# Optimization experiments

Hardware: AMD Instinct MI355X
Metric: run time of the kernel (lower is better)

The kernel has to match this reference:

```python
import jax, jax.numpy as jnp
import numpy as np

B, S, D, H, L, DFF, NA = 128, 52, 1024, 16, 8, 4096, 1000
DK = D // H
KTOP = int((1.0 - 0.9) * S)  # per-row top-k kept before threshold = 5
EPS = 1e-5
SCALE = 1.0 / np.sqrt(DK).astype(np.float32)


def setup_inputs() -> dict:
    key = jax.random.key(0)
    ks = jax.random.split(key, 30)
    # token grid: channels 0,1 in [0,50) so only designated positions match special tokens
    x = jax.random.randint(ks[0], (B, S, 3), 0, 50).astype(jnp.int32)
    act = jax.random.randint(ks[1], (B, S), 0, NA).astype(jnp.int32)
    x = x.at[..., 2].set(act)
    x = x.at[:, 0].set(jnp.array([100, 0, 1], jnp.int32))    # SOS
    x = x.at[:, 26].set(jnp.array([100, 0, 2], jnp.int32))   # SEP
    x = x.at[:, 48:].set(jnp.array([100, 0, 0], jnp.int32))  # PAD tail

    def n(k, shape, scale=0.02):
        return (jax.random.normal(k, shape) * scale).astype(jnp.float32)

    return dict(
        x=x,
        action_emb=n(ks[2], (NA, D), 1.0),
        sep_token=n(ks[3], (D,), 1.0),
        bn_gamma=jnp.ones((S,), jnp.float32),
        bn_beta=jnp.zeros((S,), jnp.float32),
        Wq=n(ks[4], (L, D, D)), bq=jnp.zeros((L, D), jnp.float32),
        Wk=n(ks[5], (L, D, D)), bk=jnp.zeros((L, D), jnp.float32),
        Wv=n(ks[6], (L, D, D)), bv=jnp.zeros((L, D), jnp.float32),
        Wo=n(ks[7], (L, D, D)), bo=jnp.zeros((L, D), jnp.float32),
        W1=n(ks[8], (L, DFF, D)), b1=jnp.zeros((L, DFF), jnp.float32),
        W2=n(ks[9], (L, D, DFF)), b2=jnp.zeros((L, D), jnp.float32),
        ln1_g=jnp.ones((L, D), jnp.float32), ln1_b=jnp.zeros((L, D), jnp.float32),
        ln2_g=jnp.ones((L, D), jnp.float32), ln2_b=jnp.zeros((L, D), jnp.float32),
        Wout=n(ks[10], (3, D)), bout=jnp.zeros((3,), jnp.float32),
    )


def _ln(x, g, b):
    m = x.mean(-1, keepdims=True)
    v = x.var(-1, keepdims=True)
    return (x - m) * jax.lax.rsqrt(v + EPS) * g + b


def reference(x, action_emb, sep_token, bn_gamma, bn_beta,
              Wq, bq, Wk, bk, Wv, bv, Wo, bo,
              W1, b1, W2, b2, ln1_g, ln1_b, ln2_g, ln2_b, Wout, bout):
    PAD = jnp.array([100, 0, 0], x.dtype)
    SEP = jnp.array([100, 0, 2], x.dtype)
    pad = jnp.all(x == PAD, -1)            # [B,S]
    sep = jnp.all(x == SEP, -1)            # [B,S]
    valid = ~pad                            # attend only to non-pad keys

    # token-scatter embedding: sep positions -> sep_token, everything else -> action embedding
    h = jnp.where(sep[..., None], sep_token, action_emb[x[..., 2]])  # [B,S,D]

    # BatchNorm1d(52) over seq-as-channel dim (training-mode batch stats)
    mu = h.mean((0, 2), keepdims=True)
    var = h.var((0, 2), keepdims=True)
    h = (h - mu) * jax.lax.rsqrt(var + EPS) * bn_gamma[None, :, None] + bn_beta[None, :, None]

    for l in range(L):
        q = (h @ Wq[l].T + bq[l]).reshape(B, S, H, DK).transpose(0, 2, 1, 3)
        k = (h @ Wk[l].T + bk[l]).reshape(B, S, H, DK).transpose(0, 2, 1, 3)
        v = (h @ Wv[l].T + bv[l]).reshape(B, S, H, DK).transpose(0, 2, 1, 3)
        scores = jnp.einsum('bhqd,bhkd->bhqk', q, k) * SCALE       # [B,H,S,S]
        scores = jnp.where(valid[:, None, None, :], scores, -1e9)
        thr = jax.lax.top_k(scores, KTOP)[0][..., -1:]              # per-row k-th largest
        sparse = scores * (scores >= thr).astype(scores.dtype)      # zero out sub-threshold
        attn = jax.nn.softmax(sparse, axis=-1)
        o = jnp.einsum('bhqk,bhkd->bhqd', attn, v).transpose(0, 2, 1, 3).reshape(B, S, D)
        o = o @ Wo[l].T + bo[l]
        h = _ln(h + o, ln1_g[l], ln1_b[l])
        f = jax.nn.relu(h @ W1[l].T + b1[l]) @ W2[l].T + b2[l]
        h = _ln(h + f, ln2_g[l], ln2_b[l])

    y = h @ Wout.T + bout                                           # [B,S,3]
    return y[:, -1]
```

## Files before the change

kernel.cpp:

```cpp
#include <hip/hip_runtime.h>
#include <cstddef>
#include <cstdint>

#define B_    128
#define S_    52
#define D_    1024
#define H_    16
#define L_    8
#define DFF_  4096
#define DK_   64
#define T_    (B_*S_)
#define EPS_  1e-5f
#define SCALE_ 0.125f

typedef unsigned short ushortx4 __attribute__((ext_vector_type(4)));
typedef short  bf16x8 __attribute__((ext_vector_type(8)));
typedef float  f32x4  __attribute__((ext_vector_type(4)));

__device__ __forceinline__ unsigned short f2b(float f) {
  unsigned int u = __builtin_bit_cast(unsigned int, f);
  u = u + 0x7fffu + ((u >> 16) & 1u);
  return (unsigned short)(u >> 16);
}
__device__ __forceinline__ float b2f(unsigned short b) {
  unsigned int u = ((unsigned int)b) << 16;
  return __builtin_bit_cast(float, u);
}
__device__ __forceinline__ void gload16(const void* g, void* l) {
  __builtin_amdgcn_global_load_lds((const __attribute__((address_space(1))) unsigned int*)g,
      (__attribute__((address_space(3))) unsigned int*)l, 16, 0, 0);
}

__global__ __launch_bounds__(256) void k_embed(const int* __restrict__ x,
    const float* __restrict__ aemb, const float* __restrict__ sept,
    float* __restrict__ h, float* __restrict__ part, int* __restrict__ mask)
{
  int row = blockIdx.x;
  int b = row / S_;
  int s = row - b * S_;
  const int* xr = x + (size_t)row * 3;
  int x0 = xr[0], x1 = xr[1], x2 = xr[2];
  bool issep = (x0 == 100) && (x1 == 0) && (x2 == 2);
  bool ispad = (x0 == 100) && (x1 == 0) && (x2 == 0);
  int t = threadIdx.x;
  if (t == 0) mask[row] = ispad ? 0 : 1;
  const float* src = issep ? sept : (aemb + (size_t)x2 * D_);
  size_t base = (size_t)row * D_;
  float s1 = 0.f, s2 = 0.f;
#pragma unroll
  for (int i = 0; i < 4; ++i) {
    int d = t + i * 256;
    float v = src[d];
    h[base + d] = v;
    s1 += v;
    s2 += v * v;
  }
#pragma unroll
  for (int off = 32; off; off >>= 1) {
    s1 += __shfl_down(s1, off);
    s2 += __shfl_down(s2, off);
  }
  __shared__ float red[8];
  int lane = t & 63, wid = t >> 6;
  if (lane == 0) { red[wid] = s1; red[4 + wid] = s2; }
  __syncthreads();
  if (t == 0) {
    part[(size_t)s * B_ + b]        = red[0] + red[1] + red[2] + red[3];
    part[(size_t)(S_ + s) * B_ + b] = red[4] + red[5] + red[6] + red[7];
  }
}

__global__ __launch_bounds__(128) void k_bn_reduce(const float* __restrict__ part,
                                                   float* __restrict__ stats)
{
  int s = blockIdx.x;
  int t = threadIdx.x;
  float s1 = part[(size_t)s * B_ + t];
  float s2 = part[(size_t)(S_ + s) * B_ + t];
#pragma unroll
  for (int off = 32; off; off >>= 1) {
    s1 += __shfl_down(s1, off);
    s2 += __shfl_down(s2, off);
  }
  __shared__ float red[4];
  int lane = t & 63, wid = t >> 6;
  if (lane == 0) { red[wid] = s1; red[2 + wid] = s2; }
  __syncthreads();
  if (t == 0) {
    stats[s]      = red[0] + red[1];
    stats[S_ + s] = red[2] + red[3];
  }
}

__global__ __launch_bounds__(256) void k_bn_apply(float* __restrict__ h,
    const float* __restrict__ stats, const float* __restrict__ g,
    const float* __restrict__ bb, unsigned short* __restrict__ hb)
{
  int row = blockIdx.x;
  int s = row % S_;
  const float cnt = (float)(B_ * D_);
  float mu  = stats[s] / cnt;
  float var = stats[S_ + s] / cnt - mu * mu;
  float sc  = rsqrtf(var + EPS_) * g[s];
  float off = bb[s] - mu * sc;
  size_t base = (size_t)row * D_;
  int t = threadIdx.x;
#pragma unroll
  for (int i = 0; i < 4; ++i) {
    int d = t + i * 256;
    float v = h[base + d] * sc + off;
    h[base + d] = v;
    hb[base + d] = f2b(v);
  }
}

__global__ __launch_bounds__(256) void k_wconv(
    const float* __restrict__ wq, const float* __restrict__ wk,
    const float* __restrict__ wv, const float* __restrict__ wo,
    const float* __restrict__ w1, const float* __restrict__ w2,
    unsigned short* __restrict__ out)
{
  const size_t DD = (size_t)D_ * D_;
  const size_t DF = (size_t)DFF_ * D_;
  const size_t total = 4 * DD + 2 * DF;
  size_t stride = (size_t)gridDim.x * 256 * 4;
  for (size_t i = ((size_t)blockIdx.x * 256 + threadIdx.x) * 4; i < total; i += stride) {
    const float* src; size_t off;
    if      (i < DD)          { src = wq; off = i; }
    else if (i < 2 * DD)      { src = wk; off = i - DD; }
    else if (i < 3 * DD)      { src = wv; off = i - 2 * DD; }
    else if (i < 4 * DD)      { src = wo; off = i - 3 * DD; }
    else if (i < 4 * DD + DF) { src = w1; off = i - 4 * DD; }
    else                      { src = w2; off = i - 4 * DD - DF; }
    float4 v = *reinterpret_cast<const float4*>(src + off);
    ushortx4 o = { f2b(v.x), f2b(v.y), f2b(v.z), f2b(v.w) };
    *reinterpret_cast<ushortx4*>(out + i) = o;
  }
}

__global__ __launch_bounds__(256) void k_bcat(const float* __restrict__ bq,
    const float* __restrict__ bk, const float* __restrict__ bv,
    float* __restrict__ out)
{
  int i = blockIdx.x * 256 + threadIdx.x;
  int l = i / 3072, j = i - l * 3072;
  float v = (j < D_) ? bq[l * D_ + j] : (j < 2 * D_) ? bk[l * D_ + j - D_]
                                                     : bv[l * D_ + j - 2 * D_];
  out[i] = v;
}

template<int RELU, int OUTBF16>
__global__ __launch_bounds__(512) void k_gemm8(
    const unsigned short* __restrict__ A, const unsigned short* __restrict__ Wt,
    const float* __restrict__ bias, void* __restrict__ C,
    int Mtiles, int Ntiles, int K, int ldc)
{
  __shared__ unsigned short lds[3 * 24576];
  const int tid = threadIdx.x;
  const int w = tid >> 6, l = tid & 63;

  const int nwg = Mtiles * Ntiles;
  int id = blockIdx.x;
  int swz = (id & 7) * (nwg >> 3) + (id >> 3);
  int bym = swz % Mtiles, bxn = swz / Mtiles;
  const int bm = bym * 256, bn = bxn * 128;

  const int srow = l >> 3;
  const unsigned inrow = ((l & 7) << 4) ^ ((l & 0x38) << 1);
  const char* gA = (const char*)A + (size_t)(bm + w * 32 + srow) * ((size_t)K * 2) + inrow;
  const char* gB = (const char*)Wt + (size_t)(bn + w * 16 + srow) * ((size_t)K * 2) + inrow;
  const size_t rj = (size_t)8 * K * 2;
  const int ldsA0 = w * 2048;
  const int ldsB0 = 16384 + w * 1024;

#define STAGE8(tt, bb) do {                                   \
    size_t kb = (size_t)(tt) * 128;                           \
    unsigned short* la = lds + (bb) * 24576 + ldsA0;          \
    unsigned short* lb = lds + (bb) * 24576 + ldsB0;          \
    gload16(gA + kb,          la);                            \
    gload16(gA + kb + rj,     la + 512);                      \
    gload16(gA + kb + 2 * rj, la + 1024);                     \
    gload16(gA + kb + 3 * rj, la + 1536);                     \
    gload16(gB + kb,          lb);                            \
    gload16(gB + kb + rj,     lb + 512);                      \
  } while (0)

  const int fr = l & 15, kg = l >> 4;
  const int wr = w >> 1, wcn = w & 1;
  const unsigned sw = (fr & 7) << 4;
  const unsigned colk0 = ((unsigned)(kg * 16)) ^ sw;
  const unsigned colk1 = ((unsigned)(64 + kg * 16)) ^ sw;
  const unsigned aRow0 = (unsigned)(wr * 64 + fr) * 128;
  const unsigned bRow0 = 32768u + (unsigned)(wcn * 64 + fr) * 128;

  f32x4 acc[4][4] = {};
  const int NT = K >> 6;

  STAGE8(0, 0);
  STAGE8(1, 1);
  asm volatile("s_waitcnt vmcnt(6)" ::: "memory");
  __builtin_amdgcn_sched_barrier(0);
  __builtin_amdgcn_s_barrier();
  __builtin_amdgcn_sched_barrier(0);

  int cur = 0;
  for (int t = 0; t < NT; ++t) {
    if (t + 2 < NT) {
      int sb = cur + 2; if (sb >= 3) sb -= 3;
      STAGE8(t + 2, sb);
    }
    const char* bp = (const char*)(lds + cur * 24576);
    bf16x8 bfr[4][2];
#pragma unroll
    for (int n = 0; n < 4; ++n) {
      bfr[n][0] = *(const bf16x8*)(bp + bRow0 + n * 2048 + colk0);
      bfr[n][1] = *(const bf16x8*)(bp + bRow0 + n * 2048 + colk1);
    }
#pragma unroll
    for (int m = 0; m < 4; ++m) {
      bf16x8 a0 = *(const bf16x8*)(bp + aRow0 + m * 2048 + colk0);
      bf16x8 a1 = *(const bf16x8*)(bp + aRow0 + m * 2048 + colk1);
#pragma unroll
      for (int n = 0; n < 4; ++n) {
        acc[m][n] = __builtin_amdgcn_mfma_f32_16x16x32_bf16(a0, bfr[n][0], acc[m][n], 0, 0, 0);
        acc[m][n] = __builtin_amdgcn_mfma_f32_16x16x32_bf16(a1, bfr[n][1], acc[m][n], 0, 0, 0);
      }
    }
    if (t + 1 < NT) {
      if (t + 2 < NT) { asm volatile("s_waitcnt vmcnt(6)" ::: "memory"); }
      else            { asm volatile("s_waitcnt vmcnt(0)" ::: "memory"); }
      __builtin_amdgcn_sched_barrier(0);
      __builtin_amdgcn_s_barrier();
      __builtin_amdgcn_sched_barrier(0);
    }
    cur = (cur == 2) ? 0 : cur + 1;
  }
#undef STAGE8

#pragma unroll
  for (int n = 0; n < 4; ++n) {
    int col = bn + wcn * 64 + n * 16 + fr;
    float bv = bias[col];
#pragma unroll
    for (int m = 0; m < 4; ++m) {
      int row0 = bm + wr * 64 + m * 16 + kg * 4;
#pragma unroll
      for (int j = 0; j < 4; ++j) {
        float v = acc[m][n][j] + bv;
        if (RELU) v = fmaxf(v, 0.f);
        if (OUTBF16)
          ((unsigned short*)C)[(size_t)(row0 + j) * ldc + col] = f2b(v);
        else
          ((float*)C)[(size_t)(row0 + j) * ldc + col] = v;
      }
    }
  }
}

__global__ __launch_bounds__(64) void k_attn(const unsigned short* __restrict__ qkv,
    const int* __restrict__ mask, unsigned short* __restrict__ ao)
{
  __shared__ float sc[64][68];
  __shared__ unsigned short ph[64][68];
  __shared__ unsigned short plo[64][68];
  __shared__ unsigned short vT[64][68];
  __shared__ float dnm[64];

  int blk = blockIdx.x;
  int b = blk >> 4, hh = blk & 15;
  int l = threadIdx.x;
  int cl = l & 15, kg = l >> 4;
  const unsigned short* base = qkv + (size_t)(b * S_) * 3072 + hh * 64;

  {
    const unsigned short* vp = base + 2048 + l;
#pragma unroll 4
    for (int k = 0; k < S_; ++k)
      vT[l][k] = vp[(size_t)k * 3072];
#pragma unroll
    for (int k = S_; k < 64; ++k) vT[l][k] = 0;
  }

  bf16x8 qa[4][2], kb[4][2];
#pragma unroll
  for (int mi = 0; mi < 4; ++mi) {
    int row = mi * 16 + cl;
    bool ok = (row < S_);
    const unsigned short* qp = base + (size_t)row * 3072 + kg * 8;
#pragma unroll
    for (int ks = 0; ks < 2; ++ks) {
      bf16x8 z = {};
      qa[mi][ks] = ok ? *reinterpret_cast<const bf16x8*>(qp + ks * 32) : z;
      kb[mi][ks] = ok ? *reinterpret_cast<const bf16x8*>(qp + 1024 + ks * 32) : z;
    }
  }

  f32x4 acc[4][4] = {};
#pragma unroll
  for (int ks = 0; ks < 2; ++ks)
#pragma unroll
    for (int mi = 0; mi < 4; ++mi)
#pragma unroll
      for (int ci = 0; ci < 4; ++ci)
        acc[mi][ci] = __builtin_amdgcn_mfma_f32_16x16x32_bf16(qa[mi][ks], kb[ci][ks], acc[mi][ci], 0, 0, 0);

  int vld[4];
#pragma unroll
  for (int ci = 0; ci < 4; ++ci) {
    int col = ci * 16 + cl;
    vld[ci] = (col < S_) ? mask[b * S_ + col] : 0;
  }
#pragma unroll
  for (int mi = 0; mi < 4; ++mi)
#pragma unroll
    for (int ci = 0; ci < 4; ++ci)
#pragma unroll
      for (int j = 0; j < 4; ++j)
        sc[mi * 16 + kg * 4 + j][ci * 16 + cl] = vld[ci] ? acc[mi][ci][j] * SCALE_ : -1e9f;

  __syncthreads();

  if (l < S_) {
    float v0 = -3e38f, v1 = -3e38f, v2 = -3e38f, v3 = -3e38f, v4 = -3e38f;
    const float4* rp = reinterpret_cast<const float4*>(&sc[l][0]);
#pragma unroll
    for (int c4 = 0; c4 < 13; ++c4) {
      float4 x = rp[c4];
      float xs[4] = { x.x, x.y, x.z, x.w };
#pragma unroll
      for (int u = 0; u < 4; ++u) {
        float xv = xs[u];
        if      (xv > v0) { v4 = v3; v3 = v2; v2 = v1; v1 = v0; v0 = xv; }
        else if (xv > v1) { v4 = v3; v3 = v2; v2 = v1; v1 = xv; }
        else if (xv > v2) { v4 = v3; v3 = v2; v2 = xv; }
        else if (xv > v3) { v4 = v3; v3 = xv; }
        else if (xv > v4) { v4 = xv; }
      }
    }
    float thr = v4;
    float m = fmaxf(v0, 0.f);
    float denom = 0.f;
    for (int c = 0; c < S_; ++c) {
      float xv = sc[l][c];
      float sp = (xv >= thr) ? xv : 0.f;
      float e = __expf(sp - m);
      denom += e;
      unsigned short hi = f2b(e);
      ph[l][c] = hi;
      plo[l][c] = f2b(e - b2f(hi));
    }
#pragma unroll
    for (int c = S_; c < 64; ++c) { ph[l][c] = 0; plo[l][c] = 0; }
    dnm[l] = 1.f / denom;
  }
  __syncthreads();

  f32x4 o[4][4] = {};
#pragma unroll
  for (int ks = 0; ks < 2; ++ks) {
    bf16x8 vf[4];
#pragma unroll
    for (int di = 0; di < 4; ++di)
      vf[di] = *reinterpret_cast<const bf16x8*>(&vT[di * 16 + cl][ks * 32 + kg * 8]);
#pragma unroll
    for (int mi = 0; mi < 4; ++mi) {
      bf16x8 ahi = *reinterpret_cast<const bf16x8*>(&ph[mi * 16 + cl][ks * 32 + kg * 8]);
      bf16x8 alo = *reinterpret_cast<const bf16x8*>(&plo[mi * 16 + cl][ks * 32 + kg * 8]);
#pragma unroll
      for (int di = 0; di < 4; ++di) {
        o[mi][di] = __builtin_amdgcn_mfma_f32_16x16x32_bf16(ahi, vf[di], o[mi][di], 0, 0, 0);
        o[mi][di] = __builtin_amdgcn_mfma_f32_16x16x32_bf16(alo, vf[di], o[mi][di], 0, 0, 0);
      }
    }
  }

#pragma unroll
  for (int mi = 0; mi < 4; ++mi) {
    int row = mi * 16 + kg * 4;
    if (row < S_) {
#pragma unroll
      for (int j = 0; j < 4; ++j) {
        int r = row + j;
        float inv = dnm[r];
        unsigned short* aop = ao + (size_t)(b * S_ + r) * D_ + hh * DK_;
#pragma unroll
        for (int di = 0; di < 4; ++di)
          aop[di * 16 + cl] = f2b(o[mi][di][j] * inv);
      }
    }
  }
}

__global__ __launch_bounds__(256) void k_add_ln(float* __restrict__ h,
    const float* __restrict__ r, const float* __restrict__ g,
    const float* __restrict__ bb, unsigned short* __restrict__ hb)
{
  int row = blockIdx.x;
  size_t base = (size_t)row * D_;
  int t = threadIdx.x;
  float xs[4];
  float s1 = 0.f, s2 = 0.f;
#pragma unroll
  for (int i = 0; i < 4; ++i) {
    int d = t + i * 256;
    float xv = h[base + d] + r[base + d];
    xs[i] = xv;
    s1 += xv;
    s2 += xv * xv;
  }
#pragma unroll
  for (int off = 32; off; off >>= 1) {
    s1 += __shfl_down(s1, off);
    s2 += __shfl_down(s2, off);
  }
  __shared__ float red[8];
  int lane = t & 63, wid = t >> 6;
  if (lane == 0) { red[wid] = s1; red[4 + wid] = s2; }
  __syncthreads();
  if (t == 0) {
    red[0] = red[0] + red[1] + red[2] + red[3];
    red[4] = red[4] + red[5] + red[6] + red[7];
  }
  __syncthreads();
  float mean = red[0] / (float)D_;
  float var  = red[4] / (float)D_ - mean * mean;
  float inv  = rsqrtf(var + EPS_);
#pragma unroll
  for (int i = 0; i < 4; ++i) {
    int d = t + i * 256;
    float v = (xs[i] - mean) * inv * g[d] + bb[d];
    h[base + d] = v;
    hb[base + d] = f2b(v);
  }
}

__global__ __launch_bounds__(256) void k_final(const float* __restrict__ h,
    const float* __restrict__ Wout, const float* __restrict__ bout,
    float* __restrict__ y)
{
  int b = blockIdx.x;
  const float* hr = h + (size_t)(b * S_ + (S_ - 1)) * D_;
  int t = threadIdx.x;
  float p0 = 0.f, p1 = 0.f, p2 = 0.f;
  for (int d = t; d < D_; d += 256) {
    float xv = hr[d];
    p0 += xv * Wout[d];
    p1 += xv * Wout[D_ + d];
    p2 += xv * Wout[2 * D_ + d];
  }
#pragma unroll
  for (int off = 32; off; off >>= 1) {
    p0 += __shfl_down(p0, off);
    p1 += __shfl_down(p1, off);
    p2 += __shfl_down(p2, off);
  }
  __shared__ float red[12];
  int lane = t & 63, wid = t >> 6;
  if (lane == 0) { red[wid] = p0; red[4 + wid] = p1; red[8 + wid] = p2; }
  __syncthreads();
  if (t == 0) {
    y[b * 3 + 0] = red[0] + red[1] + red[2]  + red[3]  + bout[0];
    y[b * 3 + 1] = red[4] + red[5] + red[6]  + red[7]  + bout[1];
    y[b * 3 + 2] = red[8] + red[9] + red[10] + red[11] + bout[2];
  }
}

extern "C" void kernel_launch(void* const* d_in, const int* in_sizes, int n_in,
                              void* d_out, int out_size, void* d_ws, size_t ws_size,
                              hipStream_t stream)
{
  const int*   x    = (const int*)d_in[0];
  const float* aemb = (const float*)d_in[1];
  const float* sept = (const float*)d_in[2];
  const float* bng  = (const float*)d_in[3];
  const float* bnb  = (const float*)d_in[4];
  const float* Wq = (const float*)d_in[5];  const float* bq = (const float*)d_in[6];
  const float* Wk = (const float*)d_in[7];  const float* bk = (const float*)d_in[8];
  const float* Wv = (const float*)d_in[9];  const float* bv = (const float*)d_in[10];
  const float* Wo = (const float*)d_in[11]; const float* bo = (const float*)d_in[12];
  const float* W1 = (const float*)d_in[13]; const float* b1 = (const float*)d_in[14];
  const float* W2 = (const float*)d_in[15]; const float* b2 = (const float*)d_in[16];
  const float* ln1g = (const float*)d_in[17]; const float* ln1b = (const float*)d_in[18];
  const float* ln2g = (const float*)d_in[19]; const float* ln2b = (const float*)d_in[20];
  const float* Wout = (const float*)d_in[21]; const float* bout = (const float*)d_in[22];
  float* out = (float*)d_out;

  float* ws = (float*)d_ws;
  const size_t TD = (size_t)T_ * D_;
  const size_t DD = (size_t)D_ * D_;
  const size_t DF = (size_t)DFF_ * D_;
  float* h   = ws;
  float* tmp = ws + TD;
  unsigned short* hb   = (unsigned short*)(ws + 2 * TD);
  unsigned short* qkvb = (unsigned short*)(ws + 2 * TD + TD / 2);
  unsigned short* aob  = (unsigned short*)(ws + 4 * TD);
  unsigned short* ffb  = (unsigned short*)(ws + 4 * TD + TD / 2);
  unsigned short* wbuf = (unsigned short*)(ws + 6 * TD + TD / 2);
  float* bqkv = ws + 6 * TD + TD / 2 + (4 * DD + 2 * DF) / 2;
  float* stats = bqkv + L_ * 3072;
  float* part  = stats + 2 * S_;
  int*   mask  = (int*)(part + 2 * S_ * B_);

  k_embed<<<T_, 256, 0, stream>>>(x, aemb, sept, h, part, mask);
  k_bn_reduce<<<S_, 128, 0, stream>>>(part, stats);
  k_bn_apply<<<T_, 256, 0, stream>>>(h, stats, bng, bnb, hb);
  k_bcat<<<(L_ * 3072) / 256, 256, 0, stream>>>(bq, bk, bv, bqkv);

  for (int l = 0; l < L_; ++l) {
    k_wconv<<<3072, 256, 0, stream>>>(Wq + l * DD, Wk + l * DD, Wv + l * DD,
                                      Wo + l * DD, W1 + l * DF, W2 + l * DF, wbuf);
    k_gemm8<0, 1><<<26 * 24, 512, 0, stream>>>(hb, wbuf, bqkv + l * 3072,
        qkvb, 26, 24, 1024, 3072);
    k_attn<<<B_ * H_, 64, 0, stream>>>(qkvb, mask, aob);
    k_gemm8<0, 0><<<26 * 8, 512, 0, stream>>>(aob, wbuf + 3 * DD, bo + l * D_,
        tmp, 26, 8, 1024, 1024);
    k_add_ln<<<T_, 256, 0, stream>>>(h, tmp, ln1g + l * D_, ln1b + l * D_, hb);
    k_gemm8<1, 1><<<26 * 32, 512, 0, stream>>>(hb, wbuf + 4 * DD, b1 + l * DFF_,
        ffb, 26, 32, 1024, 4096);
    k_gemm8<0, 0><<<26 * 8, 512, 0, stream>>>(ffb, wbuf + 4 * DD + DF, b2 + l * D_,
        tmp, 26, 8, 4096, 1024);
    k_add_ln<<<T_, 256, 0, stream>>>(h, tmp, ln2g + l * D_, ln2b + l * D_, hb);
  }
  k_final<<<B_, 256, 0, stream>>>(h, Wout, bout, out);
}
```

Measured before the change: 2.636 ms.

## Restructure GEMM pipeline into half-K phases with double-buffered LDS

Rewrites the bf16 MFMA GEMM main loop. Each 64-wide K tile is now split into two 32-wide phases, and prefetch runs three phases ahead into a double-buffered LDS (down from three full-tile buffers), with a new XOR swizzle for the 64-byte rows. Fragment loads are followed by an explicit lgkmcnt wait, and the MFMA burst is wrapped in s_setprio, to overlap global loads with compute at a finer grain and cut LDS usage. Launch bounds now state one block per CU. The tradeoffs are a barrier per half tile instead of per tile, and more intricate vmcnt bookkeeping.

Measured after the change: 2.933 ms. +11.3%, slower.

```diff
diff --git a/kernel.cpp b/kernel.cpp
--- a/kernel.cpp
+++ b/kernel.cpp
@@ -150,12 +150,12 @@
 }
 
 template<int RELU, int OUTBF16>
-__global__ __launch_bounds__(512) void k_gemm8(
+__global__ __launch_bounds__(512, 1) void k_gemm8(
     const unsigned short* __restrict__ A, const unsigned short* __restrict__ Wt,
     const float* __restrict__ bias, void* __restrict__ C,
     int Mtiles, int Ntiles, int K, int ldc)
 {
-  __shared__ unsigned short lds[3 * 24576];
+  __shared__ unsigned short lds[2 * 24576];
   const int tid = threadIdx.x;
   const int w = tid >> 6, l = tid & 63;
 
@@ -165,88 +165,80 @@
   int bym = swz % Mtiles, bxn = swz / Mtiles;
   const int bm = bym * 256, bn = bxn * 128;
 
-  const int srow = l >> 3;
-  const unsigned inrow = ((l & 7) << 4) ^ ((l & 0x38) << 1);
-  const char* gA = (const char*)A + (size_t)(bm + w * 32 + srow) * ((size_t)K * 2) + inrow;
-  const char* gB = (const char*)Wt + (size_t)(bn + w * 16 + srow) * ((size_t)K * 2) + inrow;
-  const size_t rj = (size_t)8 * K * 2;
-  const int ldsA0 = w * 2048;
-  const int ldsB0 = 16384 + w * 1024;
-
-#define STAGE8(tt, bb) do {                                   \
-    size_t kb = (size_t)(tt) * 128;                           \
-    unsigned short* la = lds + (bb) * 24576 + ldsA0;          \
-    unsigned short* lb = lds + (bb) * 24576 + ldsB0;          \
-    gload16(gA + kb,          la);                            \
-    gload16(gA + kb + rj,     la + 512);                      \
-    gload16(gA + kb + 2 * rj, la + 1024);                     \
-    gload16(gA + kb + 3 * rj, la + 1536);                     \
-    gload16(gB + kb,          lb);                            \
-    gload16(gB + kb + rj,     lb + 512);                      \
+  const int colsw = 16 * ((l & 3) ^ ((l >> 2) & 3));
+  const char* gA = (const char*)A + ((size_t)(bm + w * 16 + (l >> 2)) * K) * 2 + colsw;
+  const char* gB = (const char*)Wt + ((size_t)(bn + w * 16 + (l >> 2)) * K) * 2 + colsw;
+  const size_t rA = (size_t)128 * K * 2;
+  unsigned short* lA = lds + w * 512;
+  unsigned short* lB = lds + 16384 + w * 512;
+
+#define STAGEG(g_) do {                                         \
+    int tt_ = (g_) >> 1, kh_ = (g_) & 1, bb_ = tt_ & 1;         \
+    size_t ko_ = (size_t)tt_ * 128 + (size_t)kh_ * 64;          \
+    unsigned short* la_ = lA + bb_ * 24576 + kh_ * 8192;        \
+    unsigned short* lb_ = lB + bb_ * 24576 + kh_ * 4096;        \
+    gload16(gA + ko_,      la_);                                \
+    gload16(gA + ko_ + rA, la_ + 4096);                         \
+    gload16(gB + ko_,      lb_);                                \
   } while (0)
 
   const int fr = l & 15, kg = l >> 4;
-  const int wr = w >> 1, wcn = w & 1;
-  const unsigned sw = (fr & 7) << 4;
-  const unsigned colk0 = ((unsigned)(kg * 16)) ^ sw;
-  const unsigned colk1 = ((unsigned)(64 + kg * 16)) ^ sw;
-  const unsigned aRow0 = (unsigned)(wr * 64 + fr) * 128;
-  const unsigned bRow0 = 32768u + (unsigned)(wcn * 64 + fr) * 128;
+  const int wr = w >> 1, wc = w & 1;
+  const int xr = 16 * (kg ^ (fr & 3));
+  const int aBase = (wr * 64 + fr) * 64 + xr;
+  const int bBase = 32768 + (wc * 64 + fr) * 64 + xr;
 
   f32x4 acc[4][4] = {};
-  const int NT = K >> 6;
-
-  STAGE8(0, 0);
-  STAGE8(1, 1);
+  const int NPH = K >> 5;
+
+  STAGEG(0); STAGEG(1); STAGEG(2);
   asm volatile("s_waitcnt vmcnt(6)" ::: "memory");
   __builtin_amdgcn_sched_barrier(0);
   __builtin_amdgcn_s_barrier();
   __builtin_amdgcn_sched_barrier(0);
 
-  int cur = 0;
-  for (int t = 0; t < NT; ++t) {
-    if (t + 2 < NT) {
-      int sb = cur + 2; if (sb >= 3) sb -= 3;
-      STAGE8(t + 2, sb);
-    }
-    const char* bp = (const char*)(lds + cur * 24576);
-    bf16x8 bfr[4][2];
-#pragma unroll
-    for (int n = 0; n < 4; ++n) {
-      bfr[n][0] = *(const bf16x8*)(bp + bRow0 + n * 2048 + colk0);
-      bfr[n][1] = *(const bf16x8*)(bp + bRow0 + n * 2048 + colk1);
-    }
-#pragma unroll
-    for (int m = 0; m < 4; ++m) {
-      bf16x8 a0 = *(const bf16x8*)(bp + aRow0 + m * 2048 + colk0);
-      bf16x8 a1 = *(const bf16x8*)(bp + aRow0 + m * 2048 + colk1);
-#pragma unroll
-      for (int n = 0; n < 4; ++n) {
-        acc[m][n] = __builtin_amdgcn_mfma_f32_16x16x32_bf16(a0, bfr[n][0], acc[m][n], 0, 0, 0);
-        acc[m][n] = __builtin_amdgcn_mfma_f32_16x16x32_bf16(a1, bfr[n][1], acc[m][n], 0, 0, 0);
-      }
-    }
-    if (t + 1 < NT) {
-      if (t + 2 < NT) { asm volatile("s_waitcnt vmcnt(6)" ::: "memory"); }
-      else            { asm volatile("s_waitcnt vmcnt(0)" ::: "memory"); }
+  for (int g = 0; g < NPH; ++g) {
+    if (g + 3 < NPH) STAGEG(g + 3);
+    const char* bp = (const char*)lds + ((g >> 1) & 1) * 49152;
+    const int kh = g & 1;
+    bf16x8 af[4], bfv[4];
+#pragma unroll
+    for (int mf = 0; mf < 4; ++mf)
+      af[mf] = *(const bf16x8*)(bp + kh * 16384 + aBase + mf * 1024);
+#pragma unroll
+    for (int nf = 0; nf < 4; ++nf)
+      bfv[nf] = *(const bf16x8*)(bp + kh * 8192 + bBase + nf * 1024);
+    __builtin_amdgcn_s_setprio(1);
+    asm volatile("s_waitcnt lgkmcnt(0)" ::: "memory");
+    __builtin_amdgcn_sched_barrier(0);
+#pragma unroll
+    for (int mf = 0; mf < 4; ++mf)
+#pragma unroll
+      for (int nf = 0; nf < 4; ++nf)
+        acc[mf][nf] = __builtin_amdgcn_mfma_f32_16x16x32_bf16(af[mf], bfv[nf], acc[mf][nf], 0, 0, 0);
+    __builtin_amdgcn_s_setprio(0);
+    __builtin_amdgcn_sched_barrier(0);
+    if (g + 1 < NPH) {
+      if (g < NPH - 3)       { asm volatile("s_waitcnt vmcnt(6)" ::: "memory"); }
+      else if (g == NPH - 3) { asm volatile("s_waitcnt vmcnt(3)" ::: "memory"); }
+      else                   { asm volatile("s_waitcnt vmcnt(0)" ::: "memory"); }
       __builtin_amdgcn_sched_barrier(0);
       __builtin_amdgcn_s_barrier();
       __builtin_amdgcn_sched_barrier(0);
     }
-    cur = (cur == 2) ? 0 : cur + 1;
-  }
-#undef STAGE8
-
-#pragma unroll
-  for (int n = 0; n < 4; ++n) {
-    int col = bn + wcn * 64 + n * 16 + fr;
+  }
+#undef STAGEG
+
+#pragma unroll
+  for (int nf = 0; nf < 4; ++nf) {
+    int col = bn + wc * 64 + nf * 16 + fr;
     float bv = bias[col];
 #pragma unroll
-    for (int m = 0; m < 4; ++m) {
-      int row0 = bm + wr * 64 + m * 16 + kg * 4;
+    for (int mf = 0; mf < 4; ++mf) {
+      int row0 = bm + wr * 64 + mf * 16 + kg * 4;
 #pragma unroll
       for (int j = 0; j < 4; ++j) {
-        float v = acc[m][n][j] + bv;
+        float v = acc[mf][nf][j] + bv;
         if (RELU) v = fmaxf(v, 0.f);
         if (OUTBF16)
           ((unsigned short*)C)[(size_t)(row0 + j) * ldc + col] = f2b(v);
```
